# Performance work log

Measured on AMD Instinct MI355X. Metric: run time of the kernel, lower is better.

The kernel has to match this reference:

```python
import jax, jax.numpy as jnp
import numpy as np

B, T, C, H = 4, 2048, 1024, 16
D = C // H  # head dim 64


def setup_inputs() -> dict:
    key = jax.random.key(0)
    ks = jax.random.split(key, 5)
    std = 0.02
    return {
        "x": jax.random.normal(ks[0], (B, T, C), dtype=jnp.float32),
        "Wq": jax.random.normal(ks[1], (C, C), dtype=jnp.float32) * std,
        "bq": jnp.zeros((C,), dtype=jnp.float32),
        "Wk": jax.random.normal(ks[2], (C, C), dtype=jnp.float32) * std,
        "bk": jnp.zeros((C,), dtype=jnp.float32),
        "Wv": jax.random.normal(ks[3], (C, C), dtype=jnp.float32) * std,
        "bv": jnp.zeros((C,), dtype=jnp.float32),
        "Wp": jax.random.normal(ks[4], (C, C), dtype=jnp.float32) * std,
        "bp": jnp.zeros((C,), dtype=jnp.float32),
    }


def reference(x, Wq, bq, Wk, bk, Wv, bv, Wp, bp):
    Bsz, Tlen, Csz = x.shape
    # qkv projections -> [B, H, T, D]
    def heads(y):
        return y.reshape(Bsz, Tlen, H, D).transpose(0, 2, 1, 3)
    q = heads(x @ Wq.T + bq)
    k = heads(x @ Wk.T + bk)
    v = heads(x @ Wv.T + bv)
    scale = 1.0 / jnp.sqrt(jnp.float32(D))
    attn = jnp.einsum("bhqd,bhkd->bhqk", q, k) * scale  # [B,H,T,T]
    causal = jnp.tril(jnp.ones((Tlen, Tlen), dtype=bool))
    attn = jnp.where(causal[None, None, :, :], attn, jnp.float32(-jnp.inf))
    attn = jax.nn.softmax(attn, axis=-1)
    # dropout in eval mode: identity
    y = jnp.einsum("bhqk,bhkd->bhqd", attn, v)  # [B,H,T,D]
    y = y.transpose(0, 2, 1, 3).reshape(Bsz, Tlen, Csz)
    return y @ Wp.T + bp
```

## Files before the change

### kernel.cpp

```cpp
#include <hip/hip_runtime.h>
#include <hip/hip_bf16.h>

typedef __bf16  bf16x8 __attribute__((ext_vector_type(8)));
typedef float   f32x4  __attribute__((ext_vector_type(4)));
using bf16 = __hip_bfloat16;

#define MFMA16(A_, B_, C_) __builtin_amdgcn_mfma_f32_16x16x32_bf16((A_), (B_), (C_), 0, 0, 0)


__device__ __forceinline__ void gll16(const void* g, void* l) {
    __builtin_amdgcn_global_load_lds(
        (const __attribute__((address_space(1))) void*)g,
        (__attribute__((address_space(3))) void*)l, 16, 0, 0);
}

__device__ inline void stage8(bf16* dst, const float* src) {
    const float4 a = *(const float4*)(src);
    const float4 b = *(const float4*)(src + 4);
    union { int4 v; bf16 h[8]; } u;
    u.h[0] = __float2bfloat16(a.x); u.h[1] = __float2bfloat16(a.y);
    u.h[2] = __float2bfloat16(a.z); u.h[3] = __float2bfloat16(a.w);
    u.h[4] = __float2bfloat16(b.x); u.h[5] = __float2bfloat16(b.y);
    u.h[6] = __float2bfloat16(b.z); u.h[7] = __float2bfloat16(b.w);
    *(int4*)dst = u.v;
}
__device__ inline void stage8(bf16* dst, const bf16* src) {
    *(int4*)dst = *(const int4*)src;
}
__device__ inline void store_out(float* p, float v) { *p = v; }
__device__ inline void store_out(bf16*  p, float v) { *p = __float2bfloat16(v); }

__global__ __launch_bounds__(256) void cvt_bf16(const float* __restrict__ x,
    const float* __restrict__ W0, const float* __restrict__ W1,
    const float* __restrict__ W2, const float* __restrict__ W3,
    bf16* __restrict__ xb, bf16* __restrict__ Wb)
{
    const size_t nx4 = 2097152;
    const size_t total4 = nx4 + 4 * 262144;
    for (size_t v = (size_t)blockIdx.x * 256 + threadIdx.x; v < total4;
         v += (size_t)gridDim.x * 256) {
        const float* src; bf16* dst; size_t off;
        if (v < nx4) { src = x; dst = xb; off = v * 4; }
        else {
            const size_t vw = v - nx4;
            const int w = (int)(vw >> 18);
            off = (vw & 262143) * 4;
            src = (w == 0) ? W0 : (w == 1) ? W1 : (w == 2) ? W2 : W3;
            dst = Wb + ((size_t)w << 20);
        }
        const float4 f = *(const float4*)(src + off);
        union { bf16 h[4]; uint2 u; } pk;
        pk.h[0] = __float2bfloat16(f.x); pk.h[1] = __float2bfloat16(f.y);
        pk.h[2] = __float2bfloat16(f.z); pk.h[3] = __float2bfloat16(f.w);
        *(uint2*)(dst + off) = pk.u;
    }
}

struct GemmArgs {
    const bf16*  Bm[3];
    const float* bias[3];
    void*        out[3];
    int          mode[3];
};

__global__ __launch_bounds__(256) void gemm_bb(const bf16* __restrict__ A, GemmArgs ga)
{
    __shared__ __align__(16) bf16 sA[128 * 64];
    __shared__ __align__(16) bf16 sB[128 * 64];
    const int id  = blockIdx.x;
    const int z   = id >> 9;
    const int rem = id & 511;
    const int m0 = (rem & 63) * 128;
    const int n0 = (rem >> 6) * 128;
    const bf16*  __restrict__ Bm   = ga.Bm[z];
    const float* __restrict__ bias = ga.bias[z];
    const int mode = ga.mode[z];
    const int tid  = threadIdx.x;
    const int lane = tid & 63;
    const int wave = tid >> 6;
    const int l15  = lane & 15;
    const int quad = lane >> 4;
    const int wm = (wave >> 1) * 64;
    const int wn = (wave & 1) * 64;

    f32x4 acc[4][4] = {};

    for (int k0 = 0; k0 < 1024; k0 += 64) {
#pragma unroll
        for (int s = 0; s < 4; ++s) {
            const int L = s * 256 + tid;
            const int r = L >> 3, kl = L & 7;
            const int kg = (kl ^ (r & 7)) * 8;
            gll16(A  + (size_t)(m0 + r) * 1024 + k0 + kg, &sA[L * 8]);
            gll16(Bm + (size_t)(n0 + r) * 1024 + k0 + kg, &sB[L * 8]);
        }
        __syncthreads();

#pragma unroll
        for (int kstep = 0; kstep < 2; ++kstep) {
            const int cs = ((quad + 4 * kstep) ^ (l15 & 7)) * 8;
            bf16x8 aF[4], bF[4];
#pragma unroll
            for (int i = 0; i < 4; ++i)
                aF[i] = *(const bf16x8*)&sA[(wm + i * 16 + l15) * 64 + cs];
#pragma unroll
            for (int j = 0; j < 4; ++j)
                bF[j] = *(const bf16x8*)&sB[(wn + j * 16 + l15) * 64 + cs];
#pragma unroll
            for (int i = 0; i < 4; ++i)
#pragma unroll
                for (int j = 0; j < 4; ++j)
                    acc[i][j] = MFMA16(aF[i], bF[j], acc[i][j]);
        }
        __syncthreads();
    }

    if (mode == 2) {
        bf16* ob = (bf16*)ga.out[z];
#pragma unroll
        for (int j = 0; j < 4; ++j) {
            const int col = n0 + wn + j * 16 + l15;
            const float bv = bias[col];
            const int h = col >> 6, d = col & 63;
#pragma unroll
            for (int i = 0; i < 4; ++i) {
                const int row0 = m0 + wm + i * 16 + quad * 4;
                const int b = row0 >> 11, t = row0 & 2047;
                union { bf16 hh[4]; uint2 v; } pk;
#pragma unroll
                for (int r = 0; r < 4; ++r)
                    pk.hh[r] = __float2bfloat16(acc[i][j][r] + bv);
                *(uint2*)&ob[((size_t)(b * 16 + h) * 64 + d) * 2048 + t] = pk.v;
            }
        }
    } else if (mode == 1) {
        bf16* ob = (bf16*)ga.out[z];
#pragma unroll
        for (int j = 0; j < 4; ++j) {
            const int col = n0 + wn + j * 16 + l15;
            const float bv = bias[col];
            const int h = col >> 6, d = col & 63;
#pragma unroll
            for (int i = 0; i < 4; ++i) {
#pragma unroll
                for (int r = 0; r < 4; ++r) {
                    const int row = m0 + wm + i * 16 + quad * 4 + r;
                    const int b = row >> 11, t = row & 2047;
                    ob[((size_t)(b * 16 + h) * 2048 + t) * 64 + d] =
                        __float2bfloat16(acc[i][j][r] + bv);
                }
            }
        }
    } else {
        float* of = (float*)ga.out[z];
#pragma unroll
        for (int j = 0; j < 4; ++j) {
            const int col = n0 + wn + j * 16 + l15;
            const float bv = bias[col];
#pragma unroll
            for (int i = 0; i < 4; ++i) {
#pragma unroll
                for (int r = 0; r < 4; ++r) {
                    const int row = m0 + wm + i * 16 + quad * 4 + r;
                    of[(size_t)row * 1024 + col] = acc[i][j][r] + bv;
                }
            }
        }
    }
}

template <int MODE, typename AT, typename OT>
__global__ __launch_bounds__(256) void gemm_bt(const AT* __restrict__ A,
                                               const float* __restrict__ Bm,
                                               const float* __restrict__ bias,
                                               OT* __restrict__ Cout)
{
    __shared__ __align__(16) bf16 sA[128 * 32];
    __shared__ __align__(16) bf16 sB[128 * 32];
    const int tid  = threadIdx.x;
    const int lane = tid & 63;
    const int wave = tid >> 6;
    const int l15  = lane & 15;
    const int quad = lane >> 4;
    const int m0 = blockIdx.x * 128;
    const int n0 = blockIdx.y * 128;
    const int wm = (wave >> 1) * 64;
    const int wn = (wave & 1) * 64;

    f32x4 acc[4][4] = {};

    const int c0 = tid, c1 = tid + 256;
    const size_t aoff0 = (size_t)(m0 + (c0 >> 2)) * 1024 + (c0 & 3) * 8;
    const size_t aoff1 = (size_t)(m0 + (c1 >> 2)) * 1024 + (c1 & 3) * 8;
    const size_t boff0 = (size_t)(n0 + (c0 >> 2)) * 1024 + (c0 & 3) * 8;
    const size_t boff1 = (size_t)(n0 + (c1 >> 2)) * 1024 + (c1 & 3) * 8;

    for (int k0 = 0; k0 < 1024; k0 += 32) {
        stage8(&sA[c0 * 8], A  + aoff0 + k0);
        stage8(&sA[c1 * 8], A  + aoff1 + k0);
        stage8(&sB[c0 * 8], Bm + boff0 + k0);
        stage8(&sB[c1 * 8], Bm + boff1 + k0);
        __syncthreads();

        bf16x8 aF[4], bF[4];
#pragma unroll
        for (int i = 0; i < 4; ++i)
            aF[i] = *(const bf16x8*)&sA[(wm + i * 16 + l15) * 32 + quad * 8];
#pragma unroll
        for (int j = 0; j < 4; ++j)
            bF[j] = *(const bf16x8*)&sB[(wn + j * 16 + l15) * 32 + quad * 8];
#pragma unroll
        for (int i = 0; i < 4; ++i)
#pragma unroll
            for (int j = 0; j < 4; ++j)
                acc[i][j] = MFMA16(aF[i], bF[j], acc[i][j]);
        __syncthreads();
    }

#pragma unroll
    for (int j = 0; j < 4; ++j) {
        const int col = n0 + wn + j * 16 + l15;
        const float bv = bias[col];
#pragma unroll
        for (int i = 0; i < 4; ++i) {
#pragma unroll
            for (int r = 0; r < 4; ++r) {
                const int row = m0 + wm + i * 16 + quad * 4 + r;
                const float v = acc[i][j][r] + bv;
                size_t idx;
                if (MODE == 0) idx = (size_t)row * 1024 + col;
                else {
                    const int b = row >> 11, t = row & 2047;
                    const int h = col >> 6,  d = col & 63;
                    if (MODE == 1) idx = ((size_t)(b * 16 + h) * 2048 + t) * 64 + d;
                    else           idx = ((size_t)(b * 16 + h) * 64 + d) * 2048 + t;
                }
                store_out(&Cout[idx], v);
            }
        }
    }
}

__global__ __launch_bounds__(256) void attn_fwd4(const bf16* __restrict__ Q,
                                                 const bf16* __restrict__ K,
                                                 const bf16* __restrict__ Vt,
                                                 bf16* __restrict__ Y)
{
    __shared__ __align__(16) bf16 sK[64 * 72];
    __shared__ __align__(16) bf16 sV[64 * 72];
    __shared__ __align__(16) bf16 sP[4][16 * 72];
    const int tid  = threadIdx.x;
    const int lane = tid & 63;
    const int wave = tid >> 6;
    const int l15  = lane & 15;
    const int quad = lane >> 4;

    const int id   = blockIdx.x;
    const int sub  = id >> 3;
    const int bh   = (id & 7) * 8 + (sub >> 4);
    const int pair = sub & 15;

    const size_t headQK = (size_t)bh * 2048 * 64;
    const size_t headV  = (size_t)bh * 64 * 2048;
    const int b = bh >> 4, h = bh & 15;
    constexpr float cscale = 0.125f * 1.44269504088896340736f;

    const int c0 = tid, c1 = tid + 256;
    const int r0 = c0 >> 3, col0 = (c0 & 7) * 8;
    const int r1 = c1 >> 3, col1 = (c1 & 7) * 8;
    bf16* sPw = sP[wave];

#pragma unroll
    for (int strip = 0; strip < 2; ++strip) {
        const int qt = strip ? (31 - pair) : pair;
        const int q0 = qt * 64;
        const int myq = q0 + wave * 16 + l15;

        const bf16* qrow = Q + headQK + (size_t)myq * 64;
        const bf16x8 qF0 = *(const bf16x8*)(qrow + quad * 8);
        const bf16x8 qF1 = *(const bf16x8*)(qrow + 32 + quad * 8);

        float l_part = 0.f;
        f32x4 O[4] = {};

        for (int t0 = 0; t0 <= q0; t0 += 64) {
            *(int4*)&sK[r0 * 72 + col0] = *(const int4*)(K + headQK + (size_t)(t0 + r0) * 64 + col0);
            *(int4*)&sK[r1 * 72 + col1] = *(const int4*)(K + headQK + (size_t)(t0 + r1) * 64 + col1);
            *(int4*)&sV[r0 * 72 + col0] = *(const int4*)(Vt + headV + (size_t)r0 * 2048 + t0 + col0);
            *(int4*)&sV[r1 * 72 + col1] = *(const int4*)(Vt + headV + (size_t)r1 * 2048 + t0 + col1);
            __syncthreads();

            const bool diag = (t0 == q0);
#pragma unroll
            for (int j = 0; j < 4; ++j) {
                const bf16x8 kF0 = *(const bf16x8*)&sK[(j * 16 + l15) * 72 + quad * 8];
                const bf16x8 kF1 = *(const bf16x8*)&sK[(j * 16 + l15) * 72 + 32 + quad * 8];
                f32x4 zS = {};
                zS = MFMA16(kF0, qF0, zS);
                zS = MFMA16(kF1, qF1, zS);
                union { bf16 hh[4]; uint2 v; } pk;
#pragma unroll
                for (int r = 0; r < 4; ++r) {
                    float p = exp2f(zS[r] * cscale);
                    if (diag && (t0 + j * 16 + quad * 4 + r) > myq) p = 0.f;
                    l_part += p;
                    pk.hh[r] = __float2bfloat16(p);
                }
                *(uint2*)&sPw[l15 * 72 + j * 16 + quad * 4] = pk.v;
            }

            const bf16x8 pF0 = *(const bf16x8*)&sPw[l15 * 72 + quad * 8];
            const bf16x8 pF1 = *(const bf16x8*)&sPw[l15 * 72 + 32 + quad * 8];
#pragma unroll
            for (int jd = 0; jd < 4; ++jd) {
                const bf16x8 vF0 = *(const bf16x8*)&sV[(jd * 16 + l15) * 72 + quad * 8];
                const bf16x8 vF1 = *(const bf16x8*)&sV[(jd * 16 + l15) * 72 + 32 + quad * 8];
                O[jd] = MFMA16(vF0, pF0, O[jd]);
                O[jd] = MFMA16(vF1, pF1, O[jd]);
            }
            __syncthreads();
        }

        l_part += __shfl_xor(l_part, 16);
        l_part += __shfl_xor(l_part, 32);
        const float inv_l = 1.0f / l_part;

        bf16* yrow = Y + ((size_t)(b * 2048 + myq)) * 1024 + h * 64;
#pragma unroll
        for (int jd = 0; jd < 4; ++jd) {
            union { bf16 hh[4]; uint2 v; } ok;
#pragma unroll
            for (int r = 0; r < 4; ++r)
                ok.hh[r] = __float2bfloat16(O[jd][r] * inv_l);
            *(uint2*)&yrow[jd * 16 + quad * 4] = ok.v;
        }
    }
}

extern "C" void kernel_launch(void* const* d_in, const int* in_sizes, int n_in,
                              void* d_out, int out_size, void* d_ws, size_t ws_size,
                              hipStream_t stream)
{
    const float* x  = (const float*)d_in[0];
    const float* Wq = (const float*)d_in[1];
    const float* bq = (const float*)d_in[2];
    const float* Wk = (const float*)d_in[3];
    const float* bk = (const float*)d_in[4];
    const float* Wv = (const float*)d_in[5];
    const float* bv = (const float*)d_in[6];
    const float* Wp = (const float*)d_in[7];
    const float* bp = (const float*)d_in[8];
    float* out = (float*)d_out;
    bf16*  ws  = (bf16*)d_ws;

    constexpr size_t NE = (size_t)8192 * 1024;
    bf16* Qw = ws;
    bf16* Kw = ws + NE;
    bf16* Vw = ws + 2 * NE;
    dim3 bb(256);

    if (ws_size >= (size_t)36 * 1024 * 1024 * 2) {
        bf16* xb = ws + 3 * NE;
        bf16* Wb = ws + 4 * NE;
        bf16* Yw = xb;

        cvt_bf16<<<dim3(1024), bb, 0, stream>>>(x, Wq, Wk, Wv, Wp, xb, Wb);

        GemmArgs gq;
        gq.Bm[0] = Wb;    gq.Bm[1] = Wb + (1u << 20);  gq.Bm[2] = Wb + (2u << 20);
        gq.bias[0] = bq;  gq.bias[1] = bk;             gq.bias[2] = bv;
        gq.out[0] = Qw;   gq.out[1] = Kw;              gq.out[2] = Vw;
        gq.mode[0] = 1;   gq.mode[1] = 1;              gq.mode[2] = 2;
        gemm_bb<<<dim3(1536), bb, 0, stream>>>(xb, gq);

        attn_fwd4<<<dim3(1024), bb, 0, stream>>>(Qw, Kw, Vw, Yw);

        GemmArgs go;
        go.Bm[0] = go.Bm[1] = go.Bm[2] = Wb + ((size_t)3 << 20);
        go.bias[0] = go.bias[1] = go.bias[2] = bp;
        go.out[0] = go.out[1] = go.out[2] = out;
        go.mode[0] = go.mode[1] = go.mode[2] = 0;
        gemm_bb<<<dim3(512), bb, 0, stream>>>(Yw, go);
    } else {
        bf16* Yw = ws + 3 * NE;
        dim3 gg(64, 8);
        gemm_bt<1, float, bf16><<<gg, bb, 0, stream>>>(x, Wq, bq, Qw);
        gemm_bt<1, float, bf16><<<gg, bb, 0, stream>>>(x, Wk, bk, Kw);
        gemm_bt<2, float, bf16><<<gg, bb, 0, stream>>>(x, Wv, bv, Vw);
        attn_fwd4<<<dim3(1024), bb, 0, stream>>>(Qw, Kw, Vw, Yw);
        gemm_bt<0, bf16, float><<<gg, bb, 0, stream>>>(Yw, Wp, bp, out);
    }
}
```

Before: 283.0 us.

## Fold softmax scale into Q projection, swizzle attention LDS, MFMA row sums, split strips

Multiplies Q by the softmax scale times log2(e) in the projection epilogue, so attention can call exp2 on raw scores. Attention loads K/V through global_load_lds with XOR-swizzled unpadded LDS tiles instead of padded register-staged copies. The row sum is computed by an extra MFMA against a ones vector rather than scalar adds plus shuffles. Each block now handles one query strip (2048 blocks, longest strips first) instead of a balanced pair, which trades the built-in load balance for more parallelism and relies on the scheduler to even out work. Like before, there is no running max subtraction, so exp2 could overflow for large scores.

```diff
diff --git a/kernel.cpp b/kernel.cpp
--- a/kernel.cpp
+++ b/kernel.cpp
@@ -7,6 +7,7 @@
 
 #define MFMA16(A_, B_, C_) __builtin_amdgcn_mfma_f32_16x16x32_bf16((A_), (B_), (C_), 0, 0, 0)
 
+constexpr float CSCALE = 0.125f * 1.44269504088896340736f;
 
 __device__ __forceinline__ void gll16(const void* g, void* l) {
     __builtin_amdgcn_global_load_lds(
@@ -61,6 +62,7 @@
     const float* bias[3];
     void*        out[3];
     int          mode[3];
+    float        scale[3];
 };
 
 __global__ __launch_bounds__(256) void gemm_bb(const bf16* __restrict__ A, GemmArgs ga)
@@ -75,6 +77,7 @@
     const bf16*  __restrict__ Bm   = ga.Bm[z];
     const float* __restrict__ bias = ga.bias[z];
     const int mode = ga.mode[z];
+    const float sc = ga.scale[z];
     const int tid  = threadIdx.x;
     const int lane = tid & 63;
     const int wave = tid >> 6;
@@ -129,7 +132,7 @@
                 union { bf16 hh[4]; uint2 v; } pk;
 #pragma unroll
                 for (int r = 0; r < 4; ++r)
-                    pk.hh[r] = __float2bfloat16(acc[i][j][r] + bv);
+                    pk.hh[r] = __float2bfloat16((acc[i][j][r] + bv) * sc);
                 *(uint2*)&ob[((size_t)(b * 16 + h) * 64 + d) * 2048 + t] = pk.v;
             }
         }
@@ -147,7 +150,7 @@
                     const int row = m0 + wm + i * 16 + quad * 4 + r;
                     const int b = row >> 11, t = row & 2047;
                     ob[((size_t)(b * 16 + h) * 2048 + t) * 64 + d] =
-                        __float2bfloat16(acc[i][j][r] + bv);
+                        __float2bfloat16((acc[i][j][r] + bv) * sc);
                 }
             }
         }
@@ -173,7 +176,7 @@
 __global__ __launch_bounds__(256) void gemm_bt(const AT* __restrict__ A,
                                                const float* __restrict__ Bm,
                                                const float* __restrict__ bias,
-                                               OT* __restrict__ Cout)
+                                               OT* __restrict__ Cout, float sc)
 {
     __shared__ __align__(16) bf16 sA[128 * 32];
     __shared__ __align__(16) bf16 sB[128 * 32];
@@ -226,7 +229,7 @@
 #pragma unroll
             for (int r = 0; r < 4; ++r) {
                 const int row = m0 + wm + i * 16 + quad * 4 + r;
-                const float v = acc[i][j][r] + bv;
+                const float v = (acc[i][j][r] + bv) * sc;
                 size_t idx;
                 if (MODE == 0) idx = (size_t)row * 1024 + col;
                 else {
@@ -241,13 +244,13 @@
     }
 }
 
-__global__ __launch_bounds__(256) void attn_fwd4(const bf16* __restrict__ Q,
+__global__ __launch_bounds__(256) void attn_fwd5(const bf16* __restrict__ Q,
                                                  const bf16* __restrict__ K,
                                                  const bf16* __restrict__ Vt,
                                                  bf16* __restrict__ Y)
 {
-    __shared__ __align__(16) bf16 sK[64 * 72];
-    __shared__ __align__(16) bf16 sV[64 * 72];
+    __shared__ __align__(16) bf16 sK[64 * 64];
+    __shared__ __align__(16) bf16 sV[64 * 64];
     __shared__ __align__(16) bf16 sP[4][16 * 72];
     const int tid  = threadIdx.x;
     const int lane = tid & 63;
@@ -255,85 +258,85 @@
     const int l15  = lane & 15;
     const int quad = lane >> 4;
 
-    const int id   = blockIdx.x;
-    const int sub  = id >> 3;
-    const int bh   = (id & 7) * 8 + (sub >> 4);
-    const int pair = sub & 15;
+    const int id    = blockIdx.x;
+    const int sub   = id >> 3;
+    const int bh    = (id & 7) * 8 + (sub >> 5);
+    const int strip = 31 - (sub & 31);
+    const int q0    = strip * 64;
 
     const size_t headQK = (size_t)bh * 2048 * 64;
     const size_t headV  = (size_t)bh * 64 * 2048;
     const int b = bh >> 4, h = bh & 15;
-    constexpr float cscale = 0.125f * 1.44269504088896340736f;
-
-    const int c0 = tid, c1 = tid + 256;
-    const int r0 = c0 >> 3, col0 = (c0 & 7) * 8;
-    const int r1 = c1 >> 3, col1 = (c1 & 7) * 8;
+
+    const int myq = q0 + wave * 16 + l15;
+    const bf16* qrow = Q + headQK + (size_t)myq * 64;
+    const bf16x8 qF0 = *(const bf16x8*)(qrow + quad * 8);
+    const bf16x8 qF1 = *(const bf16x8*)(qrow + 32 + quad * 8);
+
+    bf16x8 onesF;
+#pragma unroll
+    for (int i = 0; i < 8; ++i) onesF[i] = (__bf16)1.0f;
+
+    f32x4 O[4] = {};
+    f32x4 O4  = {};
+
+    const int L0 = tid, L1 = tid + 256;
+    const int r0 = L0 >> 3, cg0 = ((L0 & 7) ^ (r0 & 7)) * 8;
+    const int r1 = L1 >> 3, cg1 = ((L1 & 7) ^ (r1 & 7)) * 8;
+    const int cs0 = (quad ^ (l15 & 7)) * 8;
+    const int cs1 = cs0 ^ 32;
     bf16* sPw = sP[wave];
 
-#pragma unroll
-    for (int strip = 0; strip < 2; ++strip) {
-        const int qt = strip ? (31 - pair) : pair;
-        const int q0 = qt * 64;
-        const int myq = q0 + wave * 16 + l15;
-
-        const bf16* qrow = Q + headQK + (size_t)myq * 64;
-        const bf16x8 qF0 = *(const bf16x8*)(qrow + quad * 8);
-        const bf16x8 qF1 = *(const bf16x8*)(qrow + 32 + quad * 8);
-
-        float l_part = 0.f;
-        f32x4 O[4] = {};
-
-        for (int t0 = 0; t0 <= q0; t0 += 64) {
-            *(int4*)&sK[r0 * 72 + col0] = *(const int4*)(K + headQK + (size_t)(t0 + r0) * 64 + col0);
-            *(int4*)&sK[r1 * 72 + col1] = *(const int4*)(K + headQK + (size_t)(t0 + r1) * 64 + col1);
-            *(int4*)&sV[r0 * 72 + col0] = *(const int4*)(Vt + headV + (size_t)r0 * 2048 + t0 + col0);
-            *(int4*)&sV[r1 * 72 + col1] = *(const int4*)(Vt + headV + (size_t)r1 * 2048 + t0 + col1);
-            __syncthreads();
-
-            const bool diag = (t0 == q0);
-#pragma unroll
-            for (int j = 0; j < 4; ++j) {
-                const bf16x8 kF0 = *(const bf16x8*)&sK[(j * 16 + l15) * 72 + quad * 8];
-                const bf16x8 kF1 = *(const bf16x8*)&sK[(j * 16 + l15) * 72 + 32 + quad * 8];
-                f32x4 zS = {};
-                zS = MFMA16(kF0, qF0, zS);
-                zS = MFMA16(kF1, qF1, zS);
-                union { bf16 hh[4]; uint2 v; } pk;
-#pragma unroll
-                for (int r = 0; r < 4; ++r) {
-                    float p = exp2f(zS[r] * cscale);
-                    if (diag && (t0 + j * 16 + quad * 4 + r) > myq) p = 0.f;
-                    l_part += p;
-                    pk.hh[r] = __float2bfloat16(p);
-                }
-                *(uint2*)&sPw[l15 * 72 + j * 16 + quad * 4] = pk.v;
-            }
-
-            const bf16x8 pF0 = *(const bf16x8*)&sPw[l15 * 72 + quad * 8];
-            const bf16x8 pF1 = *(const bf16x8*)&sPw[l15 * 72 + 32 + quad * 8];
-#pragma unroll
-            for (int jd = 0; jd < 4; ++jd) {
-                const bf16x8 vF0 = *(const bf16x8*)&sV[(jd * 16 + l15) * 72 + quad * 8];
-                const bf16x8 vF1 = *(const bf16x8*)&sV[(jd * 16 + l15) * 72 + 32 + quad * 8];
-                O[jd] = MFMA16(vF0, pF0, O[jd]);
-                O[jd] = MFMA16(vF1, pF1, O[jd]);
-            }
-            __syncthreads();
-        }
-
-        l_part += __shfl_xor(l_part, 16);
-        l_part += __shfl_xor(l_part, 32);
-        const float inv_l = 1.0f / l_part;
-
-        bf16* yrow = Y + ((size_t)(b * 2048 + myq)) * 1024 + h * 64;
+    for (int t0 = 0; t0 <= q0; t0 += 64) {
+        gll16(K  + headQK + (size_t)(t0 + r0) * 64 + cg0, &sK[L0 * 8]);
+        gll16(K  + headQK + (size_t)(t0 + r1) * 64 + cg1, &sK[L1 * 8]);
+        gll16(Vt + headV + (size_t)r0 * 2048 + t0 + cg0, &sV[L0 * 8]);
+        gll16(Vt + headV + (size_t)r1 * 2048 + t0 + cg1, &sV[L1 * 8]);
+        __syncthreads();
+
+        const bool diag = (t0 == q0);
+#pragma unroll
+        for (int j = 0; j < 4; ++j) {
+            const int row = j * 16 + l15;
+            const bf16x8 kF0 = *(const bf16x8*)&sK[row * 64 + cs0];
+            const bf16x8 kF1 = *(const bf16x8*)&sK[row * 64 + cs1];
+            f32x4 zS = {};
+            zS = MFMA16(kF0, qF0, zS);
+            zS = MFMA16(kF1, qF1, zS);
+            union { bf16 hh[4]; uint2 v; } pk;
+#pragma unroll
+            for (int r = 0; r < 4; ++r) {
+                float p = exp2f(zS[r]);
+                if (diag && (t0 + j * 16 + quad * 4 + r) > myq) p = 0.f;
+                pk.hh[r] = __float2bfloat16(p);
+            }
+            *(uint2*)&sPw[l15 * 72 + j * 16 + quad * 4] = pk.v;
+        }
+
+        const bf16x8 pF0 = *(const bf16x8*)&sPw[l15 * 72 + quad * 8];
+        const bf16x8 pF1 = *(const bf16x8*)&sPw[l15 * 72 + 32 + quad * 8];
 #pragma unroll
         for (int jd = 0; jd < 4; ++jd) {
-            union { bf16 hh[4]; uint2 v; } ok;
-#pragma unroll
-            for (int r = 0; r < 4; ++r)
-                ok.hh[r] = __float2bfloat16(O[jd][r] * inv_l);
-            *(uint2*)&yrow[jd * 16 + quad * 4] = ok.v;
-        }
+            const int vrow = jd * 16 + l15;
+            const bf16x8 vF0 = *(const bf16x8*)&sV[vrow * 64 + cs0];
+            const bf16x8 vF1 = *(const bf16x8*)&sV[vrow * 64 + cs1];
+            O[jd] = MFMA16(vF0, pF0, O[jd]);
+            O[jd] = MFMA16(vF1, pF1, O[jd]);
+        }
+        O4 = MFMA16(onesF, pF0, O4);
+        O4 = MFMA16(onesF, pF1, O4);
+        __syncthreads();
+    }
+
+    const float inv_l = 1.0f / O4[0];
+    bf16* yrow = Y + ((size_t)(b * 2048 + myq)) * 1024 + h * 64;
+#pragma unroll
+    for (int jd = 0; jd < 4; ++jd) {
+        union { bf16 hh[4]; uint2 v; } ok;
+#pragma unroll
+        for (int r = 0; r < 4; ++r)
+            ok.hh[r] = __float2bfloat16(O[jd][r] * inv_l);
+        *(uint2*)&yrow[jd * 16 + quad * 4] = ok.v;
     }
 }
 
@@ -367,27 +370,29 @@
         cvt_bf16<<<dim3(1024), bb, 0, stream>>>(x, Wq, Wk, Wv, Wp, xb, Wb);
 
         GemmArgs gq;
-        gq.Bm[0] = Wb;    gq.Bm[1] = Wb + (1u << 20);  gq.Bm[2] = Wb + (2u << 20);
-        gq.bias[0] = bq;  gq.bias[1] = bk;             gq.bias[2] = bv;
-        gq.out[0] = Qw;   gq.out[1] = Kw;              gq.out[2] = Vw;
-        gq.mode[0] = 1;   gq.mode[1] = 1;              gq.mode[2] = 2;
+        gq.Bm[0] = Wb;      gq.Bm[1] = Wb + (1u << 20);  gq.Bm[2] = Wb + (2u << 20);
+        gq.bias[0] = bq;    gq.bias[1] = bk;             gq.bias[2] = bv;
+        gq.out[0] = Qw;     gq.out[1] = Kw;              gq.out[2] = Vw;
+        gq.mode[0] = 1;     gq.mode[1] = 1;              gq.mode[2] = 2;
+        gq.scale[0] = CSCALE; gq.scale[1] = 1.0f;        gq.scale[2] = 1.0f;
         gemm_bb<<<dim3(1536), bb, 0, stream>>>(xb, gq);
 
-        attn_fwd4<<<dim3(1024), bb, 0, stream>>>(Qw, Kw, Vw, Yw);
+        attn_fwd5<<<dim3(2048), bb, 0, stream>>>(Qw, Kw, Vw, Yw);
 
         GemmArgs go;
         go.Bm[0] = go.Bm[1] = go.Bm[2] = Wb + ((size_t)3 << 20);
         go.bias[0] = go.bias[1] = go.bias[2] = bp;
         go.out[0] = go.out[1] = go.out[2] = out;
         go.mode[0] = go.mode[1] = go.mode[2] = 0;
+        go.scale[0] = go.scale[1] = go.scale[2] = 1.0f;
         gemm_bb<<<dim3(512), bb, 0, stream>>>(Yw, go);
     } else {
         bf16* Yw = ws + 3 * NE;
         dim3 gg(64, 8);
-        gemm_bt<1, float, bf16><<<gg, bb, 0, stream>>>(x, Wq, bq, Qw);
-        gemm_bt<1, float, bf16><<<gg, bb, 0, stream>>>(x, Wk, bk, Kw);
-        gemm_bt<2, float, bf16><<<gg, bb, 0, stream>>>(x, Wv, bv, Vw);
-        attn_fwd4<<<dim3(1024), bb, 0, stream>>>(Qw, Kw, Vw, Yw);
-        gemm_bt<0, bf16, float><<<gg, bb, 0, stream>>>(Yw, Wp, bp, out);
-    }
-}
+        gemm_bt<1, float, bf16><<<gg, bb, 0, stream>>>(x, Wq, bq, Qw, CSCALE);
+        gemm_bt<1, float, bf16><<<gg, bb, 0, stream>>>(x, Wk, bk, Kw, 1.0f);
+        gemm_bt<2, float, bf16><<<gg, bb, 0, stream>>>(x, Wv, bv, Vw, 1.0f);
+        attn_fwd5<<<dim3(2048), bb, 0, stream>>>(Qw, Kw, Vw, Yw);
+        gemm_bt<0, bf16, float><<<gg, bb, 0, stream>>>(Yw, Wp, bp, out, 1.0f);
+    }
+}
```

After: 298.7 us. 1.06x slower.
